# Performance work log

Measured on AMD Instinct MI355X. Metric: run time of the kernel, lower is better.

Reference implementation:

```python
import jax, jax.numpy as jnp
import numpy as np

KERNEL_SIZE = 65
STRIDE = 1
PAD = (KERNEL_SIZE - 1) // 2  # padding='same'


def setup_inputs() -> dict:
    key = jax.random.key(0)
    k1, k2 = jax.random.split(key)
    B, Cin, T = 8, 512, 512
    out_size = (Cin + 2 * PAD - (KERNEL_SIZE - 1) - 1) // STRIDE + 1  # 512
    x = jax.random.normal(k1, (B, Cin, T), dtype=jnp.float32)
    # per-output-position weights, init randn/sqrt(K) as in the torch module
    weights = jax.random.normal(k2, (out_size, 1, KERNEL_SIZE), dtype=jnp.float32) / jnp.sqrt(
        jnp.float32(KERNEL_SIZE)
    )
    bias = jnp.zeros((out_size, 1), dtype=jnp.float32)
    return {"x": x, "weights": weights, "bias": bias}


def reference(x, weights, bias):
    # x: (B, Cin, T) -> output (B, T, out_size)
    out_size, _, K = weights.shape
    xt = jnp.swapaxes(x, 1, 2)                       # (B, T, Cin)
    xp = jnp.pad(xt, ((0, 0), (0, 0), (PAD, PAD)))   # (B, T, Cin + 2p)
    # sliding windows over the (padded) channel axis: (out_size, K) gather indices
    idx = jnp.arange(out_size)[:, None] * STRIDE + jnp.arange(K)[None, :]
    win = xp[:, :, idx]                              # (B, T, out_size, K)
    # locally-connected matvec: distinct K-vector per output position o
    y = jnp.einsum("btok,ok->bto", win, weights[:, 0, :])
    y = y + bias[:, 0]                               # (B, T, out_size)
    return y
```

## Files before the change

### kernel.cpp

```cpp
#include <hip/hip_runtime.h>

#define B_    8
#define C_    512
#define T_    512
#define O_    512
#define K_    65
#define PAD_  32

#define O_TILE 32
#define T_TILE 128
#define J_     4
#define NWAVE  8
#define NTHR   512
#define ROWS   (O_TILE + 2 * PAD_)
#define NR_    (J_ + 2 * PAD_)
#define YPITCH 36

#define XTILE_ELEMS (ROWS * T_TILE)
#define WT_TILE     (NWAVE * NR_ * J_)

__global__ __launch_bounds__(NTHR, 4)
void conv_fused(const float* __restrict__ x,
                const float* __restrict__ w,
                const float* __restrict__ bias,
                float* __restrict__ out) {
    __shared__ float smem[XTILE_ELEMS + WT_TILE];
    float* xs  = smem;
    float* wts = smem + XTILE_ELEMS;

    const int tid = threadIdx.x;
    const int bid = blockIdx.x;
    const int b   = bid >> 6;
    const int rem = bid & 63;
    const int ob  = rem >> 2;
    const int tb  = rem & 3;
    const int t0  = tb * T_TILE;
    const int c_base = ob * O_TILE - PAD_;

    {
        const float* xb = x + (size_t)b * (C_ * T_);
        const int l32 = tid & 31;
        const int rg  = tid >> 5;
        #pragma unroll
        for (int rr = 0; rr < ROWS / 16; ++rr) {
            const int row = rr * 16 + rg;
            const int c   = c_base + row;
            float4 v = make_float4(0.f, 0.f, 0.f, 0.f);
            if (c >= 0 && c < C_)
                v = *(const float4*)(xb + c * T_ + t0 + l32 * 4);
            *(float4*)(&xs[row * T_TILE + l32 * 4]) = v;
        }
    }

    {
        #pragma unroll
        for (int p = 0; p < (WT_TILE + NTHR - 1) / NTHR; ++p) {
            const int e = p * NTHR + tid;
            if (e < WT_TILE) {
                const int g  = e / (NR_ * J_);
                const int r2 = e % (NR_ * J_);
                const int r  = r2 >> 2;
                const int j  = r2 & 3;
                const int o  = (ob * NWAVE + g) * J_ + j;
                const int k  = r - j;
                float v = 0.f;
                if (k >= 0 && k < K_) v = w[o * K_ + k];
                wts[e] = v;
            }
        }
    }
    __syncthreads();

    const int lane = tid & 63;
    const int wu   = __builtin_amdgcn_readfirstlane(tid >> 6);
    const int obase = ob * O_TILE + wu * J_;

    float2 acc[J_];
    #pragma unroll
    for (int j = 0; j < J_; ++j) {
        const float bj = bias[obase + j];
        acc[j] = make_float2(bj, bj);
    }

    const int tl = lane * 2;
    const float* xrow = xs + (wu * J_) * T_TILE + tl;
    const float4* wrow = (const float4*)(wts) + wu * NR_;

    #pragma unroll 4
    for (int r = 0; r < NR_; ++r) {
        const float2 xv = *(const float2*)(xrow + r * T_TILE);
        const float4 wv = wrow[r];
        acc[0].x += wv.x * xv.x;  acc[0].y += wv.x * xv.y;
        acc[1].x += wv.y * xv.x;  acc[1].y += wv.y * xv.y;
        acc[2].x += wv.z * xv.x;  acc[2].y += wv.z * xv.y;
        acc[3].x += wv.w * xv.x;  acc[3].y += wv.w * xv.y;
    }

    __syncthreads();

    *(float4*)(&smem[tl * YPITCH + wu * J_])       = make_float4(acc[0].x, acc[1].x, acc[2].x, acc[3].x);
    *(float4*)(&smem[(tl + 1) * YPITCH + wu * J_]) = make_float4(acc[0].y, acc[1].y, acc[2].y, acc[3].y);
    __syncthreads();

    {
        float* ob_out = out + (size_t)b * (T_ * O_) + (size_t)t0 * O_ + ob * O_TILE;
        const int ol   = (tid & 7) * 4;
        const int trow = tid >> 3;
        #pragma unroll
        for (int p = 0; p < 2; ++p) {
            const int t_local = p * 64 + trow;
            const float4 v = *(const float4*)(&smem[t_local * YPITCH + ol]);
            *(float4*)(ob_out + (size_t)t_local * O_ + ol) = v;
        }
    }
}

extern "C" void kernel_launch(void* const* d_in, const int* in_sizes, int n_in,
                              void* d_out, int out_size, void* d_ws, size_t ws_size,
                              hipStream_t stream) {
    const float* x    = (const float*)d_in[0];
    const float* w    = (const float*)d_in[1];
    const float* bias = (const float*)d_in[2];
    float* out = (float*)d_out;
    (void)d_ws; (void)ws_size;

    const int nblocks = B_ * (O_ / O_TILE) * (T_ / T_TILE);
    conv_fused<<<nblocks, NTHR, 0, stream>>>(x, w, bias, out);
}
```

Before: 73.41 us.

## Read x directly from global memory instead of staging tile in LDS

Drops the shared-memory staging of the 96-row x tile and has each wave load its 68 input rows straight from global memory, with a fast path that skips bounds checks when the window is fully interior. The reduced LDS footprint allows raising launch bounds to 8 blocks per CU, and the output transpose buffer gets an XOR swizzle to reduce bank conflicts, which also removes one barrier. Overlapping row windows between waves now rely on L1/L2 caching instead of LDS reuse, so global traffic per block goes up.

Result: slower. 81.40 us (+10.9%).

```diff
diff --git a/kernel.cpp b/kernel.cpp
--- a/kernel.cpp
+++ b/kernel.cpp
@@ -12,21 +12,22 @@
 #define J_     4
 #define NWAVE  8
 #define NTHR   512
-#define ROWS   (O_TILE + 2 * PAD_)
 #define NR_    (J_ + 2 * PAD_)
 #define YPITCH 36
 
-#define XTILE_ELEMS (ROWS * T_TILE)
-#define WT_TILE     (NWAVE * NR_ * J_)
+#define WT_TILE (NWAVE * NR_ * J_)
+#define YT_ELEMS (T_TILE * YPITCH)
 
-__global__ __launch_bounds__(NTHR, 4)
+#define YSWZ(row) ((((row) >> 3) & 7) << 2)
+
+__global__ __launch_bounds__(NTHR, 8)
 void conv_fused(const float* __restrict__ x,
                 const float* __restrict__ w,
                 const float* __restrict__ bias,
                 float* __restrict__ out) {
-    __shared__ float smem[XTILE_ELEMS + WT_TILE];
-    float* xs  = smem;
-    float* wts = smem + XTILE_ELEMS;
+    __shared__ float smem[WT_TILE + YT_ELEMS];
+    float* wts = smem;
+    float* ys  = smem + WT_TILE;
 
     const int tid = threadIdx.x;
     const int bid = blockIdx.x;
@@ -35,22 +36,6 @@
     const int ob  = rem >> 2;
     const int tb  = rem & 3;
     const int t0  = tb * T_TILE;
-    const int c_base = ob * O_TILE - PAD_;
-
-    {
-        const float* xb = x + (size_t)b * (C_ * T_);
-        const int l32 = tid & 31;
-        const int rg  = tid >> 5;
-        #pragma unroll
-        for (int rr = 0; rr < ROWS / 16; ++rr) {
-            const int row = rr * 16 + rg;
-            const int c   = c_base + row;
-            float4 v = make_float4(0.f, 0.f, 0.f, 0.f);
-            if (c >= 0 && c < C_)
-                v = *(const float4*)(xb + c * T_ + t0 + l32 * 4);
-            *(float4*)(&xs[row * T_TILE + l32 * 4]) = v;
-        }
-    }
 
     {
         #pragma unroll
@@ -83,23 +68,43 @@
     }
 
     const int tl = lane * 2;
-    const float* xrow = xs + (wu * J_) * T_TILE + tl;
+    const float* xg = x + (size_t)b * (C_ * T_) + t0 + tl;
     const float4* wrow = (const float4*)(wts) + wu * NR_;
+    const int c0 = obase - PAD_;
 
-    #pragma unroll 4
-    for (int r = 0; r < NR_; ++r) {
-        const float2 xv = *(const float2*)(xrow + r * T_TILE);
-        const float4 wv = wrow[r];
-        acc[0].x += wv.x * xv.x;  acc[0].y += wv.x * xv.y;
-        acc[1].x += wv.y * xv.x;  acc[1].y += wv.y * xv.y;
-        acc[2].x += wv.z * xv.x;  acc[2].y += wv.z * xv.y;
-        acc[3].x += wv.w * xv.x;  acc[3].y += wv.w * xv.y;
+    if (c0 >= 0 && c0 + NR_ - 1 < C_) {
+        #pragma unroll 4
+        for (int r = 0; r < NR_; ++r) {
+            const float2 xv = *(const float2*)(xg + (size_t)(c0 + r) * T_);
+            const float4 wv = wrow[r];
+            acc[0].x += wv.x * xv.x;  acc[0].y += wv.x * xv.y;
+            acc[1].x += wv.y * xv.x;  acc[1].y += wv.y * xv.y;
+            acc[2].x += wv.z * xv.x;  acc[2].y += wv.z * xv.y;
+            acc[3].x += wv.w * xv.x;  acc[3].y += wv.w * xv.y;
+        }
+    } else {
+        #pragma unroll 4
+        for (int r = 0; r < NR_; ++r) {
+            const int c = c0 + r;
+            float2 xv = make_float2(0.f, 0.f);
+            if (c >= 0 && c < C_)
+                xv = *(const float2*)(xg + (size_t)c * T_);
+            const float4 wv = wrow[r];
+            acc[0].x += wv.x * xv.x;  acc[0].y += wv.x * xv.y;
+            acc[1].x += wv.y * xv.x;  acc[1].y += wv.y * xv.y;
+            acc[2].x += wv.z * xv.x;  acc[2].y += wv.z * xv.y;
+            acc[3].x += wv.w * xv.x;  acc[3].y += wv.w * xv.y;
+        }
     }
 
-    __syncthreads();
-
-    *(float4*)(&smem[tl * YPITCH + wu * J_])       = make_float4(acc[0].x, acc[1].x, acc[2].x, acc[3].x);
-    *(float4*)(&smem[(tl + 1) * YPITCH + wu * J_]) = make_float4(acc[0].y, acc[1].y, acc[2].y, acc[3].y);
+    {
+        const int olb = wu * J_;
+        const int r0 = tl, r1 = tl + 1;
+        *(float4*)(&ys[r0 * YPITCH + (olb ^ YSWZ(r0))]) =
+            make_float4(acc[0].x, acc[1].x, acc[2].x, acc[3].x);
+        *(float4*)(&ys[r1 * YPITCH + (olb ^ YSWZ(r1))]) =
+            make_float4(acc[0].y, acc[1].y, acc[2].y, acc[3].y);
+    }
     __syncthreads();
 
     {
@@ -109,7 +114,7 @@
         #pragma unroll
         for (int p = 0; p < 2; ++p) {
             const int t_local = p * 64 + trow;
-            const float4 v = *(const float4*)(&smem[t_local * YPITCH + ol]);
+            const float4 v = *(const float4*)(&ys[t_local * YPITCH + (ol ^ YSWZ(t_local))]);
             *(float4*)(ob_out + (size_t)t_local * O_ + ol) = v;
         }
     }
```
